# Performance work log

Hardware: AMD Instinct MI355X
Metric: run time of the kernel (lower is better)

The kernel has to match this reference:

```python
import math
import jax, jax.numpy as jnp
import numpy as np

NUM_BUCKETS = 32
MAX_DISTANCE = 128
N_HEADS = 16
D_KV = 64


def _relative_position_bucket(rel_pos, num_buckets=NUM_BUCKETS, max_distance=MAX_DISTANCE):
    # bidirectional=True branch of T5's bucketing
    num_buckets = num_buckets // 2
    rel_buckets = (rel_pos > 0).astype(jnp.int32) * num_buckets
    rel_pos = jnp.abs(rel_pos)
    max_exact = num_buckets // 2
    is_small = rel_pos < max_exact
    # safe log (values < max_exact are masked out by is_small)
    rp_f = jnp.maximum(rel_pos, 1).astype(jnp.float32)
    rel_if_large = max_exact + (
        jnp.log(rp_f / max_exact) / math.log(max_distance / max_exact) * (num_buckets - max_exact)
    ).astype(jnp.int32)
    rel_if_large = jnp.minimum(rel_if_large, num_buckets - 1)
    return rel_buckets + jnp.where(is_small, rel_pos, rel_if_large)


def compute_bias(rel_bias_table, q_len, k_len):
    ctx = jnp.arange(q_len)[:, None]
    mem = jnp.arange(k_len)[None, :]
    buckets = _relative_position_bucket(mem - ctx)  # [q, k]
    values = rel_bias_table[buckets]                # [q, k, h]
    return jnp.transpose(values, (2, 0, 1))[None]   # [1, h, q, k]


def setup_inputs() -> dict:
    key = jax.random.key(0)
    k1, k2, k3, k4 = jax.random.split(key, 4)
    d_model = 1024
    return {
        "hidden_states": jax.random.normal(k1, (2, 2048, d_model), jnp.float32),
        "w_qkv": jax.random.normal(k2, (d_model, 3 * N_HEADS * D_KV), jnp.float32) * (d_model ** -0.5),
        "w_o": jax.random.normal(k3, (N_HEADS * D_KV, d_model), jnp.float32) * ((N_HEADS * D_KV) ** -0.5),
        "rel_bias_table": jax.random.normal(k4, (NUM_BUCKETS, N_HEADS), jnp.float32),
    }


def reference(hidden_states, w_qkv, w_o, rel_bias_table):
    b, s, _ = hidden_states.shape
    inner = N_HEADS * D_KV
    qkv = hidden_states @ w_qkv                         # [b, s, 3*inner]
    q, k, v = jnp.split(qkv, [inner, 2 * inner], axis=-1)
    def to_bhsd(x):
        return jnp.transpose(x.reshape(b, s, N_HEADS, D_KV), (0, 2, 1, 3))
    q, k, v = to_bhsd(q), to_bhsd(k), to_bhsd(v)
    scores = jnp.einsum("bhqd,bhkd->bhqk", q, k)        # no 1/sqrt(d) scaling in T5
    position_bias = compute_bias(rel_bias_table, s, s)  # [1, h, q, k]
    scores = scores + position_bias
    attn = jax.nn.softmax(scores.astype(jnp.float32), axis=-1).astype(scores.dtype)
    out = jnp.einsum("bhqk,bhkd->bhqd", attn, v)
    out = jnp.transpose(out, (0, 2, 1, 3)).reshape(b, s, inner)
    attn_output = out @ w_o
    return attn_output, position_bias
```

## Files before the change

kernel.cpp:

```cpp
#include <hip/hip_runtime.h>
#include <hip/hip_bf16.h>
#include <cstdint>
#include <cstddef>

#define S_LEN 2048
#define NH 16
#define DKV 64
#define BATCH 2
#define DMODEL 1024
#define LOG2E 1.4426950408889634f

typedef _Float16 half_t;
typedef __attribute__((ext_vector_type(4))) _Float16 halfx4;
typedef __attribute__((ext_vector_type(8))) _Float16 half8;
typedef __attribute__((ext_vector_type(4))) float floatx4;

__device__ __forceinline__ void load_lds16(const half_t* g, half_t* l) {
  __builtin_amdgcn_global_load_lds((const __attribute__((address_space(1))) void*)g,
                                   (__attribute__((address_space(3))) void*)l, 16, 0, 0);
}

__device__ __forceinline__ int t5_bucket(int delta) {
  int base = (delta > 0) ? 16 : 0;
  int a = delta < 0 ? -delta : delta;
  int n;
  if (a < 8)       n = a;
  else if (a < 12) n = 8;
  else if (a < 16) n = 9;
  else if (a < 23) n = 10;
  else if (a < 32) n = 11;
  else if (a < 46) n = 12;
  else if (a < 64) n = 13;
  else if (a < 91) n = 14;
  else             n = 15;
  return base + n;
}

__global__ __launch_bounds__(256) void bias_kernel(const float* __restrict__ table,
                                                   float* __restrict__ out) {
  int h = blockIdx.x >> 11;
  int q = blockIdx.x & (S_LEN - 1);
  __shared__ float tb[32];
  if (threadIdx.x < 32) tb[threadIdx.x] = table[threadIdx.x * NH + h];
  __syncthreads();
  float* dst = out + (size_t)blockIdx.x * S_LEN;
  int k0 = threadIdx.x * 4;
#pragma unroll
  for (int half = 0; half < 2; half++) {
    int k = k0 + half * 1024;
    float4 v;
    v.x = tb[t5_bucket((k + 0) - q)];
    v.y = tb[t5_bucket((k + 1) - q)];
    v.z = tb[t5_bucket((k + 2) - q)];
    v.w = tb[t5_bucket((k + 3) - q)];
    *(float4*)(dst + k) = v;
  }
}

__global__ __launch_bounds__(256) void cast_f2h(const float* __restrict__ in,
                                                half_t* __restrict__ out) {
  int i = blockIdx.x * 256 + threadIdx.x;
  float4 v = ((const float4*)in)[i];
  halfx4 h;
  h[0] = (half_t)v.x; h[1] = (half_t)v.y; h[2] = (half_t)v.z; h[3] = (half_t)v.w;
  ((halfx4*)out)[i] = h;
}

__global__ __launch_bounds__(256) void transpose_cast(const float* __restrict__ in,
                                                      half_t* __restrict__ out,
                                                      int R, int C) {
  __shared__ float t[32][33];
  int lr = threadIdx.x >> 3;
  int lc = (threadIdx.x & 7) * 4;
  int r0 = blockIdx.y * 32, c0 = blockIdx.x * 32;
  float4 v = *(const float4*)(in + (size_t)(r0 + lr) * C + c0 + lc);
  t[lr][lc + 0] = v.x; t[lr][lc + 1] = v.y; t[lr][lc + 2] = v.z; t[lr][lc + 3] = v.w;
  __syncthreads();
  halfx4 hv;
#pragma unroll
  for (int u = 0; u < 4; u++) hv[u] = (half_t)t[lc + u][lr];
  *(halfx4*)(out + (size_t)(c0 + lr) * R + r0 + lc) = hv;
}

__global__ __launch_bounds__(256) void vtrans(const half_t* __restrict__ V,
                                              half_t* __restrict__ Vt) {
  __shared__ half_t T[64 * 72];
  const int bh = blockIdx.y;
  const int s0 = blockIdx.x * 64;
  const half_t* src = V + ((size_t)bh * S_LEN + s0) * DKV;
  half_t* dst = Vt + (size_t)bh * DKV * S_LEN + s0;
  const int sr = threadIdx.x >> 3;
  const int dc = (threadIdx.x & 7) * 8;
#pragma unroll
  for (int p = 0; p < 2; p++) {
    int s = sr + p * 32;
    half8 v = *(const half8*)(src + (size_t)s * DKV + dc);
#pragma unroll
    for (int u = 0; u < 8; u++) T[(dc + u) * 72 + s] = v[u];
  }
  __syncthreads();
#pragma unroll
  for (int p = 0; p < 2; p++) {
    int d = sr + p * 32;
    half8 v = *(half8*)&T[d * 72 + dc];
    *(half8*)(dst + (size_t)d * S_LEN + dc) = v;
  }
}

template <int MODE>
__global__ __launch_bounds__(256) void hgemm128(const half_t* __restrict__ A,
                                                const half_t* __restrict__ Bt,
                                                float* __restrict__ C,
                                                half_t* __restrict__ Qo,
                                                half_t* __restrict__ Ko,
                                                half_t* __restrict__ Vo,
                                                int M, int N, int K) {
  __shared__ half_t Asl[8 * 512];
  __shared__ half_t Bsl[8 * 512];

  const int tid = threadIdx.x;
  const int w = tid >> 6;
  const int lane = tid & 63;
  const int l15 = lane & 15;
  const int quad = lane >> 4;
  const int wm = w >> 1, wn = w & 1;
  const int m0 = blockIdx.y * 128;
  const int n0 = blockIdx.x * 128;

  floatx4 acc[4][4];
#pragma unroll
  for (int i = 0; i < 4; i++)
#pragma unroll
    for (int j = 0; j < 4; j++) acc[i][j] = (floatx4){0.f, 0.f, 0.f, 0.f};

  const half_t* ga0 = A + (size_t)(m0 + (2 * w + 0) * 16 + l15) * K + quad * 8;
  const half_t* ga1 = A + (size_t)(m0 + (2 * w + 1) * 16 + l15) * K + quad * 8;
  const half_t* gb0 = Bt + (size_t)(n0 + (2 * w + 0) * 16 + l15) * K + quad * 8;
  const half_t* gb1 = Bt + (size_t)(n0 + (2 * w + 1) * 16 + l15) * K + quad * 8;
  half_t* la0 = &Asl[(2 * w + 0) * 512];
  half_t* la1 = &Asl[(2 * w + 1) * 512];
  half_t* lb0 = &Bsl[(2 * w + 0) * 512];
  half_t* lb1 = &Bsl[(2 * w + 1) * 512];

  for (int k0 = 0; k0 < K; k0 += 32) {
    __syncthreads();
    load_lds16(ga0 + k0, la0);
    load_lds16(ga1 + k0, la1);
    load_lds16(gb0 + k0, lb0);
    load_lds16(gb1 + k0, lb1);
    __syncthreads();

    half8 af[4], bf[4];
#pragma unroll
    for (int i = 0; i < 4; i++) af[i] = *(half8*)&Asl[(wm * 4 + i) * 512 + lane * 8];
#pragma unroll
    for (int j = 0; j < 4; j++) bf[j] = *(half8*)&Bsl[(wn * 4 + j) * 512 + lane * 8];
#pragma unroll
    for (int i = 0; i < 4; i++)
#pragma unroll
      for (int j = 0; j < 4; j++)
        acc[i][j] = __builtin_amdgcn_mfma_f32_16x16x32_f16(af[i], bf[j], acc[i][j], 0, 0, 0);
  }

  const int rowbase = m0 + wm * 64;
  const int colbase = n0 + wn * 64;
  if (MODE == 0) {
#pragma unroll
    for (int i = 0; i < 4; i++)
#pragma unroll
      for (int j = 0; j < 4; j++)
#pragma unroll
        for (int r = 0; r < 4; r++)
          C[(size_t)(rowbase + i * 16 + quad * 4 + r) * N + colbase + j * 16 + l15] =
              acc[i][j][r];
  } else {
    const int which = colbase >> 10;
    const int h = (colbase & 1023) >> 6;
    const int b = rowbase >> 11;
    const int s0 = rowbase & (S_LEN - 1);
    const float scale = (which == 0) ? LOG2E : 1.0f;
    half_t* base = ((which == 0) ? Qo : (which == 1) ? Ko : Vo) +
                   (size_t)(b * NH + h) * S_LEN * DKV;
#pragma unroll
    for (int i = 0; i < 4; i++)
#pragma unroll
      for (int j = 0; j < 4; j++)
#pragma unroll
        for (int r = 0; r < 4; r++)
          base[(size_t)(s0 + i * 16 + quad * 4 + r) * DKV + j * 16 + l15] =
              (half_t)(acc[i][j][r] * scale);
  }
}

__global__ __launch_bounds__(256) void attn_split(const half_t* __restrict__ Q,
                                                  const half_t* __restrict__ K,
                                                  const half_t* __restrict__ Vt,
                                                  const float* __restrict__ table,
                                                  float* __restrict__ Opart,
                                                  float* __restrict__ Mp,
                                                  float* __restrict__ Lp) {
  __shared__ half_t Ks[64 * 64];
  __shared__ half_t Vts[64 * 64];
  __shared__ float tb[32];
  __shared__ float badd[184];

  const int tid = threadIdx.x;
  const int w = tid >> 6;
  const int lane = tid & 63;
  const int l15 = lane & 15;
  const int quad = lane >> 4;
  const int bh = blockIdx.y;
  const int h = bh & (NH - 1);
  const int part = blockIdx.x & 1;
  const int q0w = (blockIdx.x >> 1) * 64 + w * 16;

  if (tid < 32) tb[tid] = table[tid * NH + h] * LOG2E;
  __syncthreads();
  if (tid < 183) badd[tid] = tb[t5_bucket(tid - 91)];
  const float tb_neg = tb[15], tb_pos = tb[31];

  half8 qf[2];
#pragma unroll
  for (int ks = 0; ks < 2; ks++)
    qf[ks] = *(const half8*)(Q + ((size_t)bh * S_LEN + q0w + l15) * DKV +
                             ks * 32 + quad * 8);

  floatx4 o[4];
#pragma unroll
  for (int nb = 0; nb < 4; nb++) o[nb] = (floatx4){0.f, 0.f, 0.f, 0.f};
  float m = -1e30f, l = 0.0f;

  const int jr = tid >> 2;
  const int ub = (tid & 3) * 2;
  const int sw = jr & 7;
  const int kv_rd0 = l15 * 64 + ((0 * 4 + quad) ^ (l15 & 7)) * 8;
  const int kv_rd1 = l15 * 64 + ((1 * 4 + quad) ^ (l15 & 7)) * 8;
  const int q2h = quad >> 1, q2l = (quad & 1) * 4;

  const half_t* Kg = K + ((size_t)bh * S_LEN + part * 1024 + jr) * DKV + ub * 8;
  const half_t* Vg = Vt + ((size_t)bh * DKV + jr) * S_LEN + part * 1024 + ub * 8;
  int rel = part * 1024 - q0w;

  for (int it = 0; it < 16; it++, rel += 64, Kg += 64 * DKV, Vg += 64) {
    __syncthreads();
    {
      half8 k0v = *(const half8*)(Kg);
      half8 k1v = *(const half8*)(Kg + 8);
      half8 v0v = *(const half8*)(Vg);
      half8 v1v = *(const half8*)(Vg + 8);
      *(half8*)&Ks[jr * 64 + ((ub + 0) ^ sw) * 8] = k0v;
      *(half8*)&Ks[jr * 64 + ((ub + 1) ^ sw) * 8] = k1v;
      *(half8*)&Vts[jr * 64 + ((ub + 0) ^ sw) * 8] = v0v;
      *(half8*)&Vts[jr * 64 + ((ub + 1) ^ sw) * 8] = v1v;
    }
    __syncthreads();

    floatx4 s[4];
#pragma unroll
    for (int nb = 0; nb < 4; nb++) {
      s[nb] = (floatx4){0.f, 0.f, 0.f, 0.f};
      s[nb] = __builtin_amdgcn_mfma_f32_16x16x32_f16(
          *(half8*)&Ks[nb * 1024 + kv_rd0], qf[0], s[nb], 0, 0, 0);
      s[nb] = __builtin_amdgcn_mfma_f32_16x16x32_f16(
          *(half8*)&Ks[nb * 1024 + kv_rd1], qf[1], s[nb], 0, 0, 0);
    }

    float cm = fmaxf(fmaxf(fmaxf(s[0][0], s[0][1]), fmaxf(s[0][2], s[0][3])),
                     fmaxf(fmaxf(s[1][0], s[1][1]), fmaxf(s[1][2], s[1][3])));
    cm = fmaxf(cm, fmaxf(fmaxf(fmaxf(s[2][0], s[2][1]), fmaxf(s[2][2], s[2][3])),
                         fmaxf(fmaxf(s[3][0], s[3][1]), fmaxf(s[3][2], s[3][3]))));
    {
      int i = __builtin_amdgcn_ds_swizzle(__float_as_int(cm), 0x401F);
      cm = fmaxf(cm, __int_as_float(i));
      cm = fmaxf(cm, __shfl_xor(cm, 32));
    }
    float mn = fmaxf(m, cm);
    float al = exp2f(m - mn);
    m = mn;

    float lsum = 0.0f;
    halfx4 pvb[4];
    if (rel >= 106 || rel <= -154) {
      const float sh = ((rel >= 106) ? tb_pos : tb_neg) - mn;
#pragma unroll
      for (int nb = 0; nb < 4; nb++)
#pragma unroll
        for (int r = 0; r < 4; r++) {
          float p = exp2f(s[nb][r] + sh);
          lsum += p;
          pvb[nb][r] = (half_t)p;
        }
    } else {
      const int db = rel + quad * 4 - l15 + 91;
#pragma unroll
      for (int nb = 0; nb < 4; nb++)
#pragma unroll
        for (int r = 0; r < 4; r++) {
          int idx = db + nb * 16 + r;
          idx = idx < 0 ? 0 : (idx > 182 ? 182 : idx);
          float p = exp2f(s[nb][r] - mn + badd[idx]);
          lsum += p;
          pvb[nb][r] = (half_t)p;
        }
    }
    {
      int i = __builtin_amdgcn_ds_swizzle(__float_as_int(lsum), 0x401F);
      lsum += __int_as_float(i);
      lsum += __shfl_xor(lsum, 32);
    }
    l = l * al + lsum;
#pragma unroll
    for (int nb = 0; nb < 4; nb++)
#pragma unroll
      for (int r = 0; r < 4; r++) o[nb][r] *= al;

#pragma unroll
    for (int nb = 0; nb < 4; nb++) {
      const int vrow = (nb * 16 + l15);
      const int vsw = vrow & 7;
#pragma unroll
      for (int kt = 0; kt < 4; kt++) {
        halfx4 vf = *(halfx4*)&Vts[vrow * 64 + ((kt * 2 + q2h) ^ vsw) * 8 + q2l];
        o[nb] = __builtin_amdgcn_mfma_f32_16x16x16f16(vf, pvb[kt], o[nb], 0, 0, 0);
      }
    }
  }

  {
    int row = bh * S_LEN + q0w + l15;
    float* op = Opart + (size_t)part * 4194304 + (size_t)row * 64;
#pragma unroll
    for (int nb = 0; nb < 4; nb++)
      *(float4*)(op + nb * 16 + quad * 4) =
          make_float4(o[nb][0], o[nb][1], o[nb][2], o[nb][3]);
    if (quad == 0) {
      Mp[part * 65536 + row] = m;
      Lp[part * 65536 + row] = l;
    }
  }
}

__global__ __launch_bounds__(256) void attn_combine(const float* __restrict__ Opart,
                                                    const float* __restrict__ Mp,
                                                    const float* __restrict__ Lp,
                                                    half_t* __restrict__ X) {
  int idx = blockIdx.x * 256 + threadIdx.x;
  int row = idx >> 6;
  int d = idx & 63;
  float m0 = Mp[row], m1 = Mp[65536 + row];
  float l0 = Lp[row], l1 = Lp[65536 + row];
  float M = fmaxf(m0, m1);
  float a0 = exp2f(m0 - M), a1 = exp2f(m1 - M);
  float L = l0 * a0 + l1 * a1;
  float o = (Opart[(size_t)row * 64 + d] * a0 +
             Opart[4194304 + (size_t)row * 64 + d] * a1) / L;
  int bh = row >> 11, q = row & (S_LEN - 1);
  int b = bh >> 4, h = bh & (NH - 1);
  X[(size_t)(b * S_LEN + q) * DMODEL + h * DKV + d] = (half_t)o;
}

extern "C" void kernel_launch(void* const* d_in, const int* in_sizes, int n_in,
                              void* d_out, int out_size, void* d_ws, size_t ws_size,
                              hipStream_t stream) {
  const float* hidden = (const float*)d_in[0];
  const float* w_qkv = (const float*)d_in[1];
  const float* w_o = (const float*)d_in[2];
  const float* table = (const float*)d_in[3];

  float* attn_out = (float*)d_out;
  float* bias_out = (float*)d_out + 4194304;

  half_t* Ah  = (half_t*)d_ws;
  half_t* Wqt = Ah + 4194304;
  half_t* Wot = Wqt + 3145728;
  half_t* Qh  = Wot + 1048576;
  half_t* Kh  = Qh + 4194304;
  half_t* Vh  = Kh + 4194304;
  half_t* Xh  = Vh + 4194304;
  half_t* Vth = Ah;
  float* Opart = (float*)(Xh + 4194304);
  float* Mpp   = Opart + 8388608;
  float* Lpp   = Mpp + 131072;

  cast_f2h<<<4096, 256, 0, stream>>>(hidden, Ah);
  transpose_cast<<<dim3(3072 / 32, 1024 / 32), 256, 0, stream>>>(w_qkv, Wqt, 1024, 3072);
  transpose_cast<<<dim3(1024 / 32, 1024 / 32), 256, 0, stream>>>(w_o, Wot, 1024, 1024);
  bias_kernel<<<NH * S_LEN, 256, 0, stream>>>(table, bias_out);

  hgemm128<1><<<dim3(3072 / 128, 4096 / 128), 256, 0, stream>>>(
      Ah, Wqt, nullptr, Qh, Kh, Vh, 4096, 3072, 1024);

  vtrans<<<dim3(S_LEN / 64, BATCH * NH), 256, 0, stream>>>(Vh, Vth);

  attn_split<<<dim3((S_LEN / 64) * 2, BATCH * NH), 256, 0, stream>>>(
      Qh, Kh, Vth, table, Opart, Mpp, Lpp);
  attn_combine<<<4194304 / 256, 256, 0, stream>>>(Opart, Mpp, Lpp, Xh);

  hgemm128<0><<<dim3(1024 / 128, 4096 / 128), 256, 0, stream>>>(
      Xh, Wot, attn_out, nullptr, nullptr, nullptr, 4096, 1024, 1024);
}
```

Measured before the change: 497.5 us.

## Fuse split-KV attention and combine into single 512-thread kernel with prefetch

Replaces the two-way split-KV attention plus separate combine kernel with a single kernel where each 512-thread block handles 128 queries over the full key range and writes normalized fp16 output directly. This removes the fp32 partial-output round trip through global memory and one launch. It also register-prefetches the next K/V tile while computing the current one, and skips the rescale of o and l when the running max does not change across the wavefront. In exchange the grid has half as many blocks, each running a longer serial loop, which reduces parallelism.

```diff
diff --git a/kernel.cpp b/kernel.cpp
--- a/kernel.cpp
+++ b/kernel.cpp
@@ -192,13 +192,11 @@
   }
 }
 
-__global__ __launch_bounds__(256) void attn_split(const half_t* __restrict__ Q,
+__global__ __launch_bounds__(512) void attn_fused(const half_t* __restrict__ Q,
                                                   const half_t* __restrict__ K,
                                                   const half_t* __restrict__ Vt,
                                                   const float* __restrict__ table,
-                                                  float* __restrict__ Opart,
-                                                  float* __restrict__ Mp,
-                                                  float* __restrict__ Lp) {
+                                                  half_t* __restrict__ X) {
   __shared__ half_t Ks[64 * 64];
   __shared__ half_t Vts[64 * 64];
   __shared__ float tb[32];
@@ -211,8 +209,7 @@
   const int quad = lane >> 4;
   const int bh = blockIdx.y;
   const int h = bh & (NH - 1);
-  const int part = blockIdx.x & 1;
-  const int q0w = (blockIdx.x >> 1) * 64 + w * 16;
+  const int q0w = blockIdx.x * 128 + w * 16;
 
   if (tid < 32) tb[tid] = table[tid * NH + h] * LOG2E;
   __syncthreads();
@@ -230,30 +227,31 @@
   for (int nb = 0; nb < 4; nb++) o[nb] = (floatx4){0.f, 0.f, 0.f, 0.f};
   float m = -1e30f, l = 0.0f;
 
-  const int jr = tid >> 2;
-  const int ub = (tid & 3) * 2;
-  const int sw = jr & 7;
+  const int jr = tid >> 3;
+  const int u = tid & 7;
+  const int swu = (u ^ (jr & 7)) * 8;
   const int kv_rd0 = l15 * 64 + ((0 * 4 + quad) ^ (l15 & 7)) * 8;
   const int kv_rd1 = l15 * 64 + ((1 * 4 + quad) ^ (l15 & 7)) * 8;
   const int q2h = quad >> 1, q2l = (quad & 1) * 4;
 
-  const half_t* Kg = K + ((size_t)bh * S_LEN + part * 1024 + jr) * DKV + ub * 8;
-  const half_t* Vg = Vt + ((size_t)bh * DKV + jr) * S_LEN + part * 1024 + ub * 8;
-  int rel = part * 1024 - q0w;
-
-  for (int it = 0; it < 16; it++, rel += 64, Kg += 64 * DKV, Vg += 64) {
+  const half_t* Kg = K + ((size_t)bh * S_LEN + jr) * DKV + u * 8;
+  const half_t* Vg = Vt + ((size_t)bh * DKV + jr) * S_LEN + u * 8;
+  int rel = -q0w;
+
+  half8 kreg = *(const half8*)Kg;
+  half8 vreg = *(const half8*)Vg;
+
+  for (int it = 0; it < 32; it++, rel += 64) {
     __syncthreads();
-    {
-      half8 k0v = *(const half8*)(Kg);
-      half8 k1v = *(const half8*)(Kg + 8);
-      half8 v0v = *(const half8*)(Vg);
-      half8 v1v = *(const half8*)(Vg + 8);
-      *(half8*)&Ks[jr * 64 + ((ub + 0) ^ sw) * 8] = k0v;
-      *(half8*)&Ks[jr * 64 + ((ub + 1) ^ sw) * 8] = k1v;
-      *(half8*)&Vts[jr * 64 + ((ub + 0) ^ sw) * 8] = v0v;
-      *(half8*)&Vts[jr * 64 + ((ub + 1) ^ sw) * 8] = v1v;
-    }
+    *(half8*)&Ks[jr * 64 + swu] = kreg;
+    *(half8*)&Vts[jr * 64 + swu] = vreg;
     __syncthreads();
+    if (it < 31) {
+      Kg += 64 * DKV;
+      Vg += 64;
+      kreg = *(const half8*)Kg;
+      vreg = *(const half8*)Vg;
+    }
 
     floatx4 s[4];
 #pragma unroll
@@ -275,8 +273,15 @@
       cm = fmaxf(cm, __shfl_xor(cm, 32));
     }
     float mn = fmaxf(m, cm);
-    float al = exp2f(m - mn);
-    m = mn;
+    if (!__all(cm <= m)) {
+      float al = exp2f(m - mn);
+      l *= al;
+#pragma unroll
+      for (int nb = 0; nb < 4; nb++)
+#pragma unroll
+        for (int r = 0; r < 4; r++) o[nb][r] *= al;
+      m = mn;
+    }
 
     float lsum = 0.0f;
     halfx4 pvb[4];
@@ -308,11 +313,7 @@
       lsum += __int_as_float(i);
       lsum += __shfl_xor(lsum, 32);
     }
-    l = l * al + lsum;
-#pragma unroll
-    for (int nb = 0; nb < 4; nb++)
-#pragma unroll
-      for (int r = 0; r < 4; r++) o[nb][r] *= al;
+    l += lsum;
 
 #pragma unroll
     for (int nb = 0; nb < 4; nb++) {
@@ -327,36 +328,17 @@
   }
 
   {
-    int row = bh * S_LEN + q0w + l15;
-    float* op = Opart + (size_t)part * 4194304 + (size_t)row * 64;
-#pragma unroll
-    for (int nb = 0; nb < 4; nb++)
-      *(float4*)(op + nb * 16 + quad * 4) =
-          make_float4(o[nb][0], o[nb][1], o[nb][2], o[nb][3]);
-    if (quad == 0) {
-      Mp[part * 65536 + row] = m;
-      Lp[part * 65536 + row] = l;
-    }
-  }
-}
-
-__global__ __launch_bounds__(256) void attn_combine(const float* __restrict__ Opart,
-                                                    const float* __restrict__ Mp,
-                                                    const float* __restrict__ Lp,
-                                                    half_t* __restrict__ X) {
-  int idx = blockIdx.x * 256 + threadIdx.x;
-  int row = idx >> 6;
-  int d = idx & 63;
-  float m0 = Mp[row], m1 = Mp[65536 + row];
-  float l0 = Lp[row], l1 = Lp[65536 + row];
-  float M = fmaxf(m0, m1);
-  float a0 = exp2f(m0 - M), a1 = exp2f(m1 - M);
-  float L = l0 * a0 + l1 * a1;
-  float o = (Opart[(size_t)row * 64 + d] * a0 +
-             Opart[4194304 + (size_t)row * 64 + d] * a1) / L;
-  int bh = row >> 11, q = row & (S_LEN - 1);
-  int b = bh >> 4, h = bh & (NH - 1);
-  X[(size_t)(b * S_LEN + q) * DMODEL + h * DKV + d] = (half_t)o;
+    const float inv = 1.0f / l;
+    const int b = bh >> 4;
+    half_t* xp = X + (size_t)(b * S_LEN + q0w + l15) * DMODEL + h * DKV;
+#pragma unroll
+    for (int nb = 0; nb < 4; nb++) {
+      halfx4 hv;
+#pragma unroll
+      for (int r = 0; r < 4; r++) hv[r] = (half_t)(o[nb][r] * inv);
+      *(halfx4*)(xp + nb * 16 + quad * 4) = hv;
+    }
+  }
 }
 
 extern "C" void kernel_launch(void* const* d_in, const int* in_sizes, int n_in,
@@ -378,9 +360,6 @@
   half_t* Vh  = Kh + 4194304;
   half_t* Xh  = Vh + 4194304;
   half_t* Vth = Ah;
-  float* Opart = (float*)(Xh + 4194304);
-  float* Mpp   = Opart + 8388608;
-  float* Lpp   = Mpp + 131072;
 
   cast_f2h<<<4096, 256, 0, stream>>>(hidden, Ah);
   transpose_cast<<<dim3(3072 / 32, 1024 / 32), 256, 0, stream>>>(w_qkv, Wqt, 1024, 3072);
@@ -392,9 +371,8 @@
 
   vtrans<<<dim3(S_LEN / 64, BATCH * NH), 256, 0, stream>>>(Vh, Vth);
 
-  attn_split<<<dim3((S_LEN / 64) * 2, BATCH * NH), 256, 0, stream>>>(
-      Qh, Kh, Vth, table, Opart, Mpp, Lpp);
-  attn_combine<<<4194304 / 256, 256, 0, stream>>>(Opart, Mpp, Lpp, Xh);
+  attn_fused<<<dim3(S_LEN / 128, BATCH * NH), 512, 0, stream>>>(
+      Qh, Kh, Vth, table, Xh);
 
   hgemm128<0><<<dim3(1024 / 128, 4096 / 128), 256, 0, stream>>>(
       Xh, Wot, attn_out, nullptr, nullptr, nullptr, 4096, 1024, 1024);
```

After: 487.4 us. 1.02x faster.
